# Kernel tuning notes

Measured on AMD Instinct MI355X. Metric: run time of the kernel, lower is better.

Reference implementation:

```python
import jax, jax.numpy as jnp
import numpy as np

N = 20000      # nodes / tokens
H = 256        # hidden_size
NH = 8         # num_heads
HD = NH * H    # num_heads * hidden_size = 2048
EPS = 1e-5


def setup_inputs() -> dict:
    key = jax.random.key(0)
    ks = jax.random.split(key, 24)

    def lin_w(k, i, o):
        # xavier-ish scale for a Linear weight stored as [in, out]
        return jax.random.normal(k, (i, o), jnp.float32) * (1.0 / np.sqrt(i))

    inp = {
        'q': jax.random.normal(ks[0], (N, H), jnp.float32),
        'k': jax.random.normal(ks[1], (N, H), jnp.float32),
        'v': jax.random.normal(ks[2], (N, H), jnp.float32),
        'layer': 1,
        'Wq1': lin_w(ks[3], H, HD), 'bq1': jnp.zeros((HD,), jnp.float32),
        'Wk1': lin_w(ks[4], H, HD), 'bk1': jnp.zeros((HD,), jnp.float32),
        'Wq2': lin_w(ks[5], H, HD), 'bq2': jnp.zeros((HD,), jnp.float32),
        'Wk2': lin_w(ks[6], H, HD), 'bk2': jnp.zeros((HD,), jnp.float32),
        'Wv':  lin_w(ks[7], H, HD), 'bv':  jnp.zeros((HD,), jnp.float32),
        'ln_g': jnp.ones((HD,), jnp.float32),
        'ln_b': jnp.zeros((HD,), jnp.float32),
        'Wo': lin_w(ks[8], HD, H), 'bo': jnp.zeros((H,), jnp.float32),
        'lq1': jax.random.normal(ks[9], (H,), jnp.float32) * 0.1,
        'lk1': jax.random.normal(ks[10], (H,), jnp.float32) * 0.1,
        'lq2': jax.random.normal(ks[11], (H,), jnp.float32) * 0.1,
        'lk2': jax.random.normal(ks[12], (H,), jnp.float32) * 0.1,
    }
    return inp


def reference(q, k, v, layer, Wq1, bq1, Wk1, bk1, Wq2, bq2, Wk2, bk2,
              Wv, bv, ln_g, ln_b, Wo, bo, lq1, lk1, lq2, lk2):
    # projections: [N, H] -> [N, HD]
    q1 = q @ Wq1 + bq1
    k1 = k @ Wk1 + bk1
    q2 = q @ Wq2 + bq2
    k2 = k @ Wk2 + bk2
    vv = v @ Wv + bv

    # linear attention: K^T V -> [HD, HD]  (dropout is identity in eval mode)
    k1v = k1.T @ vv
    k2v = k2.T @ vv

    # lambda gating (scalars)
    lam1 = jnp.exp(jnp.sum(lq1 * lk1))
    lam2 = jnp.exp(jnp.sum(lq2 * lk2))
    lam_init = 0.8 - 0.6 * jnp.exp(jnp.asarray(-0.3 * layer, jnp.float32))
    lam_full = lam1 - lam2 + lam_init

    # Q @ (K^T V), differential subtraction: [N, HD]
    x = q1 @ k1v - lam_full * (q2 @ k2v)

    # LayerNorm over last dim (biased variance, eps=1e-5, like torch)
    mu = jnp.mean(x, axis=-1, keepdims=True)
    var = jnp.mean(jnp.square(x - mu), axis=-1, keepdims=True)
    x = (x - mu) / jnp.sqrt(var + EPS) * ln_g + ln_b

    x = x * (1.0 - lam_init)
    return x @ Wo + bo  # [N, H]
```

## Files before the change

### kernel.cpp

```cpp
#include <hip/hip_runtime.h>
#include <stdint.h>

typedef __bf16 bf16x8 __attribute__((ext_vector_type(8)));
typedef __bf16 bf16x4v __attribute__((ext_vector_type(4)));
typedef float f32x4 __attribute__((ext_vector_type(4)));
typedef float f32x2 __attribute__((ext_vector_type(2)));
typedef unsigned short u16x4 __attribute__((ext_vector_type(4)));
typedef unsigned short u16x8 __attribute__((ext_vector_type(8)));

#define NTOK 20000
#define NTP  20480
#define HIW  256
#define HD   2048
#define LDKP 66
#define LDS2 72

static __device__ __forceinline__ float bf2f(unsigned short h) {
  union { unsigned u; float f; } c; c.u = ((unsigned)h) << 16;
  return c.f;
}
static __device__ __forceinline__ unsigned short fbits(float x) {
  __bf16 h = (__bf16)x;
  return __builtin_bit_cast(unsigned short, h);
}

#define WRED(x) { x += __shfl_xor(x,32); x += __shfl_xor(x,16); x += __shfl_xor(x,8); \
                  x += __shfl_xor(x,4);  x += __shfl_xor(x,2);  x += __shfl_xor(x,1); }


__global__ __launch_bounds__(256) void k_front(
    const float* __restrict__ kk, const float* __restrict__ vv,
    const float* __restrict__ Wq1, const float* __restrict__ Wk1,
    const float* __restrict__ Wq2, const float* __restrict__ Wk2,
    const float* __restrict__ lq1, const float* __restrict__ lk1,
    const float* __restrict__ lq2, const float* __restrict__ lk2,
    const float* __restrict__ bq1, const float* __restrict__ bk1,
    const float* __restrict__ bq2, const float* __restrict__ bk2,
    const int* __restrict__ layer,
    unsigned short* __restrict__ kT, unsigned short* __restrict__ vT,
    float* __restrict__ skp, float* __restrict__ svp,
    unsigned short* __restrict__ Pc_part, float* __restrict__ scal) {
  __shared__ float SMEM[64][260];
  const int b = blockIdx.x, t = threadIdx.x;

  if (b < 640) {
    const int tile = b >> 1, m = b & 1;
    const float* src = m ? vv : kk;
    unsigned short* dstT = m ? vT : kT;
    float* sump = m ? svp : skp;
    #pragma unroll
    for (int i = 0; i < 16; ++i) {
      int ch = i * 256 + t;
      int row = ch >> 6, c4 = (ch & 63) * 4;
      int gtok = tile * 64 + row;
      f32x4 val = {0.f, 0.f, 0.f, 0.f};
      if (gtok < NTOK) val = *(const f32x4*)&src[(size_t)gtok * HIW + c4];
      *(f32x4*)&SMEM[row][c4] = val;
    }
    __syncthreads();
    float sum = 0.f;
    unsigned short cv[64];
    #pragma unroll
    for (int tok = 0; tok < 64; ++tok) {
      float x = SMEM[tok][t];
      sum += x;
      cv[tok] = fbits(x);
    }
    sump[tile * 256 + t] = sum;
    size_t base = (size_t)t * NTP + tile * 64;
    #pragma unroll
    for (int s = 0; s < 8; ++s)
      *(u16x8*)&dstT[base + s * 8] = *(const u16x8*)&cv[s * 8];
  } else if (b < 768) {
    unsigned short* Ak = (unsigned short*)SMEM;
    unsigned short* Bk = Ak + 128 * LDKP;
    const int idx = b - 640;
    const int pair = idx >> 6, rem = idx & 63;
    const int z = rem & 15, by = (rem >> 4) & 1, bx = (rem >> 5) & 1;
    const int i0 = bx * 128, j0 = by * 128;
    const int lane = t & 63, wave = t >> 6;
    const int wr = (wave >> 1) * 64, wc = (wave & 1) * 64;
    const int r15 = lane & 15, kg = (lane >> 4) * 8;
    const float* Wa = pair ? Wq2 : Wq1;
    const float* Wb = pair ? Wk2 : Wk1;
    f32x4 acc[4][4];
    #pragma unroll
    for (int m = 0; m < 4; ++m)
      #pragma unroll
      for (int n = 0; n < 4; ++n) acc[m][n] = (f32x4){0.f, 0.f, 0.f, 0.f};
    const int srow = t >> 1, sh = (t & 1) * 32;
    for (int kt = 0; kt < 2; ++kt) {
      const int kb = z * 128 + kt * 64 + sh;
      __syncthreads();
      #pragma unroll
      for (int c = 0; c < 8; ++c) {
        f32x4 a = *(const f32x4*)&Wa[(size_t)(i0 + srow) * HD + kb + c * 4];
        f32x4 bb = *(const f32x4*)&Wb[(size_t)(j0 + srow) * HD + kb + c * 4];
        bf16x4v oa, ob;
        #pragma unroll
        for (int u = 0; u < 4; ++u) { oa[u] = (__bf16)a[u]; ob[u] = (__bf16)bb[u]; }
        *(bf16x4v*)&Ak[srow * LDKP + sh + c * 4] = oa;
        *(bf16x4v*)&Bk[srow * LDKP + sh + c * 4] = ob;
      }
      __syncthreads();
      #pragma unroll
      for (int ks = 0; ks < 2; ++ks) {
        const int ko = ks * 32 + kg;
        bf16x8 ah[4], bh[4];
        #pragma unroll
        for (int m = 0; m < 4; ++m)
          ah[m] = *(const bf16x8*)&Ak[(wr + m * 16 + r15) * LDKP + ko];
        #pragma unroll
        for (int n = 0; n < 4; ++n)
          bh[n] = *(const bf16x8*)&Bk[(wc + n * 16 + r15) * LDKP + ko];
        #pragma unroll
        for (int m = 0; m < 4; ++m)
          #pragma unroll
          for (int n = 0; n < 4; ++n)
            acc[m][n] = __builtin_amdgcn_mfma_f32_16x16x32_bf16(ah[m], bh[n], acc[m][n], 0, 0, 0);
      }
    }
    const int rg = (lane >> 4) * 4;
    unsigned short* Pp = Pc_part + (size_t)(pair * 16 + z) * 65536;
    #pragma unroll
    for (int m = 0; m < 4; ++m)
      #pragma unroll
      for (int n = 0; n < 4; ++n)
        #pragma unroll
        for (int r = 0; r < 4; ++r)
          Pp[(i0 + wr + m * 16 + rg + r) * 256 + (j0 + wc + n * 16 + r15)] = fbits(acc[m][n][r]);
  } else {
    float* red = (float*)SMEM;
    float p1 = lq1[t] * lk1[t], p2 = lq2[t] * lk2[t];
    float d1 = 0.f, d2 = 0.f;
    #pragma unroll
    for (int u = 0; u < 8; ++u) {
      d1 += bq1[t * 8 + u] * bk1[t * 8 + u];
      d2 += bq2[t * 8 + u] * bk2[t * 8 + u];
    }
    WRED(p1); WRED(p2); WRED(d1); WRED(d2);
    int w = t >> 6;
    if ((t & 63) == 0) { red[w] = p1; red[4 + w] = p2; red[8 + w] = d1; red[12 + w] = d2; }
    __syncthreads();
    if (t == 0) {
      float s1 = red[0] + red[1] + red[2] + red[3];
      float s2 = red[4] + red[5] + red[6] + red[7];
      float dd1 = red[8] + red[9] + red[10] + red[11];
      float dd2 = red[12] + red[13] + red[14] + red[15];
      float li = 0.8f - 0.6f * expf(-0.3f * (float)layer[0]);
      float lam = expf(s1) - expf(s2) + li;
      scal[0] = lam; scal[1] = -lam; scal[2] = 1.0f - li; scal[3] = li;
      scal[4] = dd1 - lam * dd2;
    }
  }
}

__global__ __launch_bounds__(512) void k_mid(
    const unsigned short* __restrict__ kT, const unsigned short* __restrict__ vT,
    float* __restrict__ S, const unsigned short* __restrict__ Pc_part,
    const float* __restrict__ skp, const float* __restrict__ svp,
    float* __restrict__ Pc, float* __restrict__ sk, float* __restrict__ sv,
    const float* __restrict__ Wk1, const float* __restrict__ Wk2,
    const float* __restrict__ Wq1, const float* __restrict__ Wq2,
    const float* __restrict__ bq1, const float* __restrict__ bq2,
    const float* __restrict__ bk1, const float* __restrict__ bk2,
    const float* __restrict__ scal, float* __restrict__ gc, float* __restrict__ uc) {
  __shared__ unsigned short SB[2 * 2 * 128 * LDS2];
  const int b = blockIdx.x, t = threadIdx.x;

  if (b < 256) {
    const int z = b & 63, by = (b >> 6) & 1, bx = (b >> 7) & 1;
    const int i0 = bx * 128, j0 = by * 128;
    const int tok0 = z * 320;
    const int lane = t & 63, wave = t >> 6;
    const int wr = (wave >> 1) * 32, wc = (wave & 1) * 64;
    const int r15 = lane & 15, kg = (lane >> 4) * 8;
    const int m = t >> 8;
    const int local = t & 255;
    const int row2 = local >> 1;
    const int koff = (local & 1) * 32;
    const unsigned short* srcT = m ? vT : kT;
    const size_t rbase = (size_t)((m ? j0 : i0) + row2) * NTP + tok0 + koff;
    const int lds_off = m * 128 * LDS2 + row2 * LDS2 + koff;

    f32x4 acc[2][4];
    #pragma unroll
    for (int mm = 0; mm < 2; ++mm)
      #pragma unroll
      for (int n = 0; n < 4; ++n) acc[mm][n] = (f32x4){0.f, 0.f, 0.f, 0.f};
    u16x8 rA[4], rB[4];

#define LOADT(R, KT)                                                          \
    { _Pragma("unroll")                                                       \
      for (int c = 0; c < 4; ++c)                                             \
        R[c] = *(const u16x8*)&srcT[rbase + (KT) * 64 + c * 8]; }
#define WRITET(BUF, R)                                                        \
    { unsigned short* d = &SB[(BUF) * 2 * 128 * LDS2 + lds_off];              \
      _Pragma("unroll")                                                       \
      for (int c = 0; c < 4; ++c) *(u16x8*)&d[c * 8] = R[c]; }

    LOADT(rA, 0)
    WRITET(0, rA)
    LOADT(rB, 1)
    asm volatile("s_waitcnt lgkmcnt(0)" ::: "memory");
    __builtin_amdgcn_s_barrier();

    #pragma unroll
    for (int kt = 0; kt < 5; ++kt) {
      const unsigned short* Ab = &SB[(kt & 1) * 2 * 128 * LDS2];
      const unsigned short* Bb = Ab + 128 * LDS2;
      __builtin_amdgcn_s_setprio(1);
      #pragma unroll
      for (int ks = 0; ks < 2; ++ks) {
        const int ko = ks * 32 + kg;
        bf16x8 ah[2], bh[4];
        #pragma unroll
        for (int mm = 0; mm < 2; ++mm)
          ah[mm] = *(const bf16x8*)&Ab[(wr + mm * 16 + r15) * LDS2 + ko];
        #pragma unroll
        for (int n = 0; n < 4; ++n)
          bh[n] = *(const bf16x8*)&Bb[(wc + n * 16 + r15) * LDS2 + ko];
        #pragma unroll
        for (int mm = 0; mm < 2; ++mm)
          #pragma unroll
          for (int n = 0; n < 4; ++n)
            acc[mm][n] = __builtin_amdgcn_mfma_f32_16x16x32_bf16(ah[mm], bh[n], acc[mm][n], 0, 0, 0);
      }
      __builtin_amdgcn_s_setprio(0);
      if (kt < 4) {
        if ((kt & 1) == 0) {
          WRITET(1, rB)
          if (kt + 2 <= 4) LOADT(rA, kt + 2)
        } else {
          WRITET(0, rA)
          if (kt + 2 <= 4) LOADT(rB, kt + 2)
        }
      }
      asm volatile("s_waitcnt lgkmcnt(0)" ::: "memory");
      __builtin_amdgcn_s_barrier();
    }
#undef LOADT
#undef WRITET
    const int rg = (lane >> 4) * 4;
    #pragma unroll
    for (int mm = 0; mm < 2; ++mm)
      #pragma unroll
      for (int n = 0; n < 4; ++n)
        #pragma unroll
        for (int r = 0; r < 4; ++r)
          atomicAdd(&S[(i0 + wr + mm * 16 + rg + r) * 256 + (j0 + wc + n * 16 + r15)],
                    acc[mm][n][r]);
  } else if (b < 288) {
    if (t < 256) {
      size_t idx = (size_t)(b - 256) * 2048 + t * 8;
      float s1[8] = {}, s2[8] = {};
      #pragma unroll 2
      for (int z = 0; z < 16; ++z) {
        u16x8 ha = *(const u16x8*)&Pc_part[(size_t)z * 65536 + idx];
        u16x8 hb = *(const u16x8*)&Pc_part[(size_t)(16 + z) * 65536 + idx];
        #pragma unroll
        for (int u = 0; u < 8; ++u) { s1[u] += bf2f(ha[u]); s2[u] += bf2f(hb[u]); }
      }
      float lam = scal[0];
      #pragma unroll
      for (int u = 0; u < 8; ++u) Pc[idx + u] = s1[u] - lam * s2[u];
    }
  } else if (b < 290) {
    if (t < 256) {
      const float* src = (b == 288) ? skp : svp;
      float s = 0.f;
      for (int z = 0; z < 320; ++z) s += src[z * 256 + t];
      if (b == 288) sk[t] = s; else sv[t] = s;
    }
  } else {
    if (t < 256) {
      int bb = b - 290, lane = t & 63, w = t >> 6;
      bool dogc = bb < 16;
      const float* A1 = dogc ? Wk1 : Wq1;
      const float* A2 = dogc ? Wk2 : Wq2;
      const float* x1 = dogc ? bq1 : bk1;
      const float* x2 = dogc ? bq2 : bk2;
      float* outv = dogc ? gc : uc;
      float lam = scal[0];
      int rb = (bb & 15) * 16 + w * 4;
      for (int q2 = 0; q2 < 4; ++q2) {
        int row = rb + q2;
        float s1 = 0.f, s2 = 0.f;
        #pragma unroll
        for (int c = 0; c < 8; ++c) {
          int kk2 = c * 256 + lane * 4;
          f32x4 a1 = *(const f32x4*)&A1[(size_t)row * HD + kk2];
          f32x4 a2 = *(const f32x4*)&A2[(size_t)row * HD + kk2];
          f32x4 v1 = *(const f32x4*)&x1[kk2];
          f32x4 v2 = *(const f32x4*)&x2[kk2];
          #pragma unroll
          for (int u = 0; u < 4; ++u) { s1 += a1[u] * v1[u]; s2 += a2[u] * v2[u]; }
        }
        WRED(s1); WRED(s2);
        if (lane == 0) outv[row] = s1 - lam * s2;
      }
    }
  }
}

__global__ __launch_bounds__(256) void k_ac(
    const float* __restrict__ Pc, const float* __restrict__ S,
    const float* __restrict__ gc, const float* __restrict__ sk,
    float* __restrict__ Ac, float* __restrict__ tc, float* __restrict__ rv,
    float* __restrict__ scal) {
  int b = blockIdx.x, t = threadIdx.x;
  if (b < 32) {
    __shared__ float Pt[32][68];
    __shared__ float St[64][68];
    int i0 = (b >> 2) * 32, j0 = (b & 3) * 64;
    int ti = t >> 5, tj = t & 31;
    float acc[4][2] = {};
    for (int kt = 0; kt < 256; kt += 64) {
      __syncthreads();
      {
        int rr = t >> 3, c8 = (t & 7) * 8;
        *(f32x4*)&Pt[rr][c8] = *(const f32x4*)&Pc[(i0 + rr) * 256 + kt + c8];
        *(f32x4*)&Pt[rr][c8 + 4] = *(const f32x4*)&Pc[(i0 + rr) * 256 + kt + c8 + 4];
      }
      {
        int rr = t >> 2, c16 = (t & 3) * 16;
        #pragma unroll
        for (int c = 0; c < 4; ++c)
          *(f32x4*)&St[rr][c16 + c * 4] = *(const f32x4*)&S[(kt + rr) * 256 + j0 + c16 + c * 4];
      }
      __syncthreads();
      #pragma unroll 8
      for (int k2 = 0; k2 < 64; ++k2) {
        float a[4];
        #pragma unroll
        for (int u = 0; u < 4; ++u) a[u] = Pt[ti * 4 + u][k2];
        f32x2 b2 = *(const f32x2*)&St[k2][tj * 2];
        #pragma unroll
        for (int u = 0; u < 4; ++u) { acc[u][0] += a[u] * b2[0]; acc[u][1] += a[u] * b2[1]; }
      }
    }
    #pragma unroll
    for (int u = 0; u < 4; ++u) {
      Ac[(i0 + ti * 4 + u) * 256 + j0 + tj * 2] = acc[u][0];
      Ac[(i0 + ti * 4 + u) * 256 + j0 + tj * 2 + 1] = acc[u][1];
    }
  } else if (b == 32) {
    int lane = t & 63, w = t >> 6;
    f32x4 sk4 = *(const f32x4*)&sk[lane * 4];
    for (int ii = 0; ii < 64; ++ii) {
      int i = w * 64 + ii;
      f32x4 p4 = *(const f32x4*)&Pc[i * 256 + lane * 4];
      float s = p4[0] * sk4[0] + p4[1] * sk4[1] + p4[2] * sk4[2] + p4[3] * sk4[3];
      WRED(s);
      if (lane == 0) tc[i] = s;
    }
  } else {
    float s0 = 0.f, s1 = 0.f, s2 = 0.f, s3 = 0.f;
    #pragma unroll 4
    for (int i = 0; i < 256; i += 4) {
      s0 += gc[i] * S[i * 256 + t];
      s1 += gc[i + 1] * S[(i + 1) * 256 + t];
      s2 += gc[i + 2] * S[(i + 2) * 256 + t];
      s3 += gc[i + 3] * S[(i + 3) * 256 + t];
    }
    rv[t] = (s0 + s1) + (s2 + s3);
    if (t < 64) {
      f32x4 g4 = *(const f32x4*)&gc[t * 4];
      f32x4 sk4 = *(const f32x4*)&sk[t * 4];
      float a = g4[0] * sk4[0] + g4[1] * sk4[1] + g4[2] * sk4[2] + g4[3] * sk4[3];
      WRED(a);
      if (t == 0) scal[5] = a;
    }
  }
}

__global__ __launch_bounds__(256) void k_gc(
    const float* __restrict__ Ac, const float* __restrict__ Wv,
    const float* __restrict__ tc, const float* __restrict__ uc,
    const float* __restrict__ sv, const float* __restrict__ rv,
    const float* __restrict__ bv, const float* __restrict__ scal,
    float* __restrict__ Gc, float* __restrict__ cc) {
  __shared__ float At[64][68];
  __shared__ float Bt[64][132];
  __shared__ float svr[256], rvr[256];
  int t = threadIdx.x;
  int i0 = blockIdx.x * 64, j0 = blockIdx.y * 128;
  int ti = t >> 5, tj = t & 31;
  svr[t] = sv[t]; rvr[t] = rv[t];
  float acc[8][4] = {};
  f32x4 swa = {0.f, 0.f, 0.f, 0.f}, sca = {0.f, 0.f, 0.f, 0.f};
  for (int kt = 0; kt < 256; kt += 64) {
    __syncthreads();
    {
      int rr = t >> 2, c16 = (t & 3) * 16;
      #pragma unroll
      for (int c = 0; c < 4; ++c)
        *(f32x4*)&At[rr][c16 + c * 4] = *(const f32x4*)&Ac[(i0 + rr) * 256 + kt + c16 + c * 4];
    }
    {
      int rr = t >> 2, c32 = (t & 3) * 32;
      #pragma unroll
      for (int c = 0; c < 8; ++c)
        *(f32x4*)&Bt[rr][c32 + c * 4] = *(const f32x4*)&Wv[(size_t)(kt + rr) * HD + j0 + c32 + c * 4];
    }
    __syncthreads();
    #pragma unroll 8
    for (int k2 = 0; k2 < 64; ++k2) {
      float a[8];
      #pragma unroll
      for (int u = 0; u < 8; ++u) a[u] = At[ti * 8 + u][k2];
      f32x4 b = *(const f32x4*)&Bt[k2][tj * 4];
      float svk = svr[kt + k2], rvk = rvr[kt + k2];
      swa += b * svk; sca += b * rvk;
      #pragma unroll
      for (int u = 0; u < 8; ++u)
        #pragma unroll
        for (int v = 0; v < 4; ++v) acc[u][v] += a[u] * b[v];
    }
  }
  int j = j0 + tj * 4;
  f32x4 bv4 = *(const f32x4*)&bv[j];
  f32x4 wnb;
  #pragma unroll
  for (int v = 0; v < 4; ++v) wnb[v] = swa[v] + 20000.0f * bv4[v];
  if (blockIdx.x == 0 && ti == 0) {
    float ac = scal[5], dc = scal[4];
    f32x4 ccv;
    #pragma unroll
    for (int v = 0; v < 4; ++v) ccv[v] = sca[v] + ac * bv4[v] + dc * wnb[v];
    *(f32x4*)&cc[j] = ccv;
  }
  #pragma unroll
  for (int u = 0; u < 8; ++u) {
    int i = i0 + ti * 8 + u;
    float tci = tc[i], uci = uc[i];
    f32x4 o;
    #pragma unroll
    for (int v = 0; v < 4; ++v)
      o[v] = acc[u][v] + tci * bv4[v] + uci * wnb[v];
    *(f32x4*)&Gc[(size_t)i * HD + j] = o;
  }
}

__global__ __launch_bounds__(256) void k_post(
    const float* __restrict__ Gc, const float* __restrict__ cc,
    const float* __restrict__ Wo, const float* __restrict__ g,
    const float* __restrict__ lnb, const float* __restrict__ scal_c,
    unsigned short* __restrict__ Bt2, float* __restrict__ M_part,
    float* __restrict__ Hc_part, float* __restrict__ scal) {
  __shared__ float SMEM[8768];
  int b = blockIdx.x, t = threadIdx.x;
  if (b < 17) {
    int lane = t & 63, w = t >> 6;
    if (b < 16) {
      int rb = b * 16 + w * 4;
      for (int q2 = 0; q2 < 4; ++q2) {
        int row = rb + q2;
        float s1 = 0.f, s2 = 0.f;
        #pragma unroll
        for (int c = 0; c < 8; ++c) {
          int kk2 = c * 256 + lane * 4;
          f32x4 g4 = *(const f32x4*)&Gc[(size_t)row * HD + kk2];
          f32x4 c4v = *(const f32x4*)&cc[kk2];
          #pragma unroll
          for (int u = 0; u < 4; ++u) { s1 += g4[u]; s2 += g4[u] * c4v[u]; }
        }
        WRED(s1); WRED(s2);
        if (lane == 0) {
          int base = ((256 + (row >> 5)) * 64 + ((row >> 3) & 3) * 16) * 8 + (row & 7);
          Bt2[base] = fbits(s1 * (1.0f / 2048.0f));
          Bt2[base + 8] = fbits(s2);
        }
      }
    } else {
      float s1 = 0.f, s2 = 0.f;
      #pragma unroll
      for (int c = 0; c < 2; ++c) {
        f32x4 v = *(const f32x4*)&cc[t * 8 + c * 4];
        #pragma unroll
        for (int u = 0; u < 4; ++u) { s1 += v[u]; s2 += v[u] * v[u]; }
      }
      WRED(s1); WRED(s2);
      if ((t & 63) == 0) { SMEM[t >> 6] = s1; SMEM[4 + (t >> 6)] = s2; }
      __syncthreads();
      if (t == 0) {
        scal[6] = SMEM[4] + SMEM[5] + SMEM[6] + SMEM[7];
        scal[7] = (SMEM[0] + SMEM[1] + SMEM[2] + SMEM[3]) * (1.0f / 2048.0f);
      }
      for (int idx = t; idx < 14 * 256; idx += 256) {
        int ci = idx >> 8, kk2 = idx & 255;
        int col = 514 + ci;
        Bt2[((256 + (kk2 >> 5)) * 64 + ((kk2 >> 3) & 3) * 16 + (col & 15)) * 8 + (kk2 & 7)] = 0;
      }
    }
  } else if (b < 81) {
    float (*Gi)[68] = (float(*)[68])SMEM;
    float (*Gj)[69] = (float(*)[69])(SMEM + 64 * 68);
    int idx = b - 17;
    int bx = idx & 3, by = (idx >> 2) & 3, z = idx >> 4;
    int i0 = bx * 64, j0 = by * 64;
    int ti = t >> 5, tj = t & 31;
    float acc[8][2] = {};
    for (int kt = 0; kt < 512; kt += 64) {
      int kb = z * 512 + kt;
      __syncthreads();
      {
        int rr = t >> 2, c16 = (t & 3) * 16;
        #pragma unroll
        for (int c = 0; c < 4; ++c) {
          *(f32x4*)&Gi[rr][c16 + c * 4] = *(const f32x4*)&Gc[(size_t)(i0 + rr) * HD + kb + c16 + c * 4];
          *(f32x4*)&Gj[rr][c16 + c * 4] = *(const f32x4*)&Gc[(size_t)(j0 + rr) * HD + kb + c16 + c * 4];
        }
      }
      __syncthreads();
      #pragma unroll 8
      for (int k2 = 0; k2 < 64; ++k2) {
        float a[8];
        #pragma unroll
        for (int u = 0; u < 8; ++u) a[u] = Gi[ti * 8 + u][k2];
        float b0 = Gj[tj * 2][k2], b1 = Gj[tj * 2 + 1][k2];
        #pragma unroll
        for (int u = 0; u < 8; ++u) { acc[u][0] += a[u] * b0; acc[u][1] += a[u] * b1; }
      }
    }
    #pragma unroll
    for (int u = 0; u < 8; ++u) {
      M_part[(size_t)z * 65536 + (i0 + ti * 8 + u) * 256 + j0 + tj * 2] = acc[u][0];
      M_part[(size_t)z * 65536 + (i0 + ti * 8 + u) * 256 + j0 + tj * 2 + 1] = acc[u][1];
    }
  } else {
    float (*At)[68] = (float(*)[68])SMEM;
    float (*Bt)[68] = (float(*)[68])(SMEM + 32 * 68);
    int idx = b - 81;
    int bx = idx % 9, rem = idx / 9, by = rem & 3, z = rem >> 2;
    int i0 = bx * 32, j0 = by * 64;
    float s2 = scal_c[2];
    int ti = t >> 5, tj = t & 31;
    float acc[4][2] = {};
    for (int kt = 0; kt < 512; kt += 64) {
      int kb = z * 512 + kt;
      __syncthreads();
      {
        int rr = t >> 3, c8 = (t & 7) * 8, gi = i0 + rr;
        #pragma unroll
        for (int h = 0; h < 8; h += 4) {
          f32x4 g4 = *(const f32x4*)&g[kb + c8 + h];
          f32x4 a;
          if (gi < 256) {
            f32x4 gg = *(const f32x4*)&Gc[(size_t)gi * HD + kb + c8 + h];
            #pragma unroll
            for (int u = 0; u < 4; ++u) a[u] = gg[u] * g4[u];
          } else if (gi == 256) {
            a = g4;
          } else if (gi == 257) {
            f32x4 c4v = *(const f32x4*)&cc[kb + c8 + h];
            #pragma unroll
            for (int u = 0; u < 4; ++u) a[u] = c4v[u] * g4[u];
          } else if (gi == 258) {
            a = *(const f32x4*)&lnb[kb + c8 + h];
          } else {
            a = (f32x4){0.f, 0.f, 0.f, 0.f};
          }
          *(f32x4*)&At[rr][c8 + h] = a;
        }
      }
      {
        int rr = t >> 2, c16 = (t & 3) * 16;
        #pragma unroll
        for (int c = 0; c < 4; ++c) {
          f32x4 bb = *(const f32x4*)&Wo[(size_t)(kb + rr) * 256 + j0 + c16 + c * 4];
          #pragma unroll
          for (int u = 0; u < 4; ++u) bb[u] *= s2;
          *(f32x4*)&Bt[rr][c16 + c * 4] = bb;
        }
      }
      __syncthreads();
      #pragma unroll 8
      for (int k2 = 0; k2 < 64; ++k2) {
        float a[4];
        #pragma unroll
        for (int u = 0; u < 4; ++u) a[u] = At[ti * 4 + u][k2];
        f32x2 b2 = *(const f32x2*)&Bt[k2][tj * 2];
        #pragma unroll
        for (int u = 0; u < 4; ++u) { acc[u][0] += a[u] * b2[0]; acc[u][1] += a[u] * b2[1]; }
      }
    }
    #pragma unroll
    for (int u = 0; u < 4; ++u) {
      Hc_part[(size_t)z * 73728 + (i0 + ti * 4 + u) * 256 + j0 + tj * 2] = acc[u][0];
      Hc_part[(size_t)z * 73728 + (i0 + ti * 4 + u) * 256 + j0 + tj * 2 + 1] = acc[u][1];
    }
  }
}

__global__ __launch_bounds__(256) void k_red2(
    const float* __restrict__ M_part, const float* __restrict__ Hc_part,
    const float* __restrict__ bo, unsigned short* __restrict__ Bt2,
    float* __restrict__ wbar, float* __restrict__ hcv, float* __restrict__ bcv) {
  int bi = blockIdx.x, z2 = blockIdx.y, t = threadIdx.x;
  if (z2 == 2) {
    if (bi != 0) return;
    float s0 = 0.f, s1 = 0.f, s2 = 0.f;
    #pragma unroll
    for (int z = 0; z < 4; ++z) {
      s0 += Hc_part[(size_t)z * 73728 + 256 * 256 + t];
      s1 += Hc_part[(size_t)z * 73728 + 257 * 256 + t];
      s2 += Hc_part[(size_t)z * 73728 + 258 * 256 + t];
    }
    wbar[t] = s0; hcv[t] = s1; bcv[t] = s2 + bo[t];
    return;
  }
  __shared__ unsigned short T[64][256];
  const float* src = z2 ? Hc_part : M_part;
  const size_t sp = z2 ? 73728 : 65536;
  const int base = z2 ? 256 : 0;
  for (int ii = 0; ii < 64; ++ii) {
    int i = bi * 64 + ii;
    float s = 0.f;
    #pragma unroll
    for (int z = 0; z < 4; ++z) s += src[z * sp + i * 256 + t];
    T[ii][t] = fbits(s);
  }
  __syncthreads();
  const int col = base + t;
  #pragma unroll
  for (int c = 0; c < 64; c += 8) {
    u16x8 o;
    #pragma unroll
    for (int u = 0; u < 8; ++u) o[u] = T[c + u][t];
    int kk0 = bi * 64 + c;
    int addr = (((col >> 4) * 8 + (kk0 >> 5)) * 64 + ((kk0 >> 3) & 3) * 16 + (col & 15)) * 8;
    *(u16x8*)&Bt2[addr] = o;
  }
}

__global__ __launch_bounds__(256) void k_out(
    const float* __restrict__ q, const unsigned short* __restrict__ Bt2,
    const float* __restrict__ hcv, const float* __restrict__ wbar,
    const float* __restrict__ bcv, const float* __restrict__ scal,
    float* __restrict__ out) {
  __shared__ unsigned short As[32 * 264];
  __shared__ float sqp[2][32];
  __shared__ float muL[32], m2L[32];
  const int t = threadIdx.x, lane = t & 63, wave = t >> 6;
  const int row0 = blockIdx.x * 32;
  const int r15 = lane & 15, kg = lane >> 4;
  {
    int r = t >> 3;
    #pragma unroll
    for (int ci = 0; ci < 8; ++ci) {
      int col = ci * 32 + (t & 7) * 4;
      f32x4 v = *(const f32x4*)&q[(size_t)(row0 + r) * HIW + col];
      bf16x4v o;
      #pragma unroll
      for (int u = 0; u < 4; ++u) o[u] = (__bf16)v[u];
      *(bf16x4v*)&As[r * 264 + col] = o;
    }
  }
  __syncthreads();
  const int wc = wave * 128;
  const unsigned short* bbase = Bt2 + (size_t)(wave * 8) * 4096 + (size_t)lane * 8;
  f32x4 acc[2][9];
  #pragma unroll
  for (int m = 0; m < 2; ++m)
    #pragma unroll
    for (int n = 0; n < 9; ++n) acc[m][n] = (f32x4){0.f, 0.f, 0.f, 0.f};
  __builtin_amdgcn_s_setprio(1);
  #pragma unroll
  for (int ko = 0; ko < 8; ++ko) {
    bf16x8 af0 = *(const bf16x8*)&As[r15 * 264 + ko * 32 + kg * 8];
    bf16x8 af1 = *(const bf16x8*)&As[(16 + r15) * 264 + ko * 32 + kg * 8];
    #pragma unroll
    for (int ni = 0; ni < 9; ++ni) {
      if (ni == 8 && wave != 3) continue;
      bf16x8 bfr = *(const bf16x8*)&bbase[ni * 4096 + ko * 512];
      acc[0][ni] = __builtin_amdgcn_mfma_f32_16x16x32_bf16(af0, bfr, acc[0][ni], 0, 0, 0);
      acc[1][ni] = __builtin_amdgcn_mfma_f32_16x16x32_bf16(af1, bfr, acc[1][ni], 0, 0, 0);
    }
  }
  __builtin_amdgcn_s_setprio(0);
  if (wave < 2) {
    #pragma unroll
    for (int m = 0; m < 2; ++m)
      #pragma unroll
      for (int r = 0; r < 4; ++r) {
        int rowl = m * 16 + kg * 4 + r;
        float p = 0.f;
        #pragma unroll
        for (int ni = 0; ni < 8; ++ni) {
          int col = wc + ni * 16 + r15;
          p += acc[m][ni][r] * bf2f(As[rowl * 264 + col]);
        }
        p += __shfl_xor(p, 1); p += __shfl_xor(p, 2);
        p += __shfl_xor(p, 4); p += __shfl_xor(p, 8);
        if (r15 == 0) sqp[wave][rowl] = p;
      }
  }
  if (wave == 3) {
    #pragma unroll
    for (int m = 0; m < 2; ++m)
      #pragma unroll
      for (int r = 0; r < 4; ++r) {
        int rowl = m * 16 + kg * 4 + r;
        if (r15 == 0) muL[rowl] = acc[m][8][r];
        if (r15 == 1) m2L[rowl] = acc[m][8][r];
      }
  }
  __syncthreads();
  if (wave >= 2) {
    const float css = scal[6], cbar = scal[7];
    #pragma unroll
    for (int m = 0; m < 2; ++m)
      #pragma unroll
      for (int r = 0; r < 4; ++r) {
        int rowl = m * 16 + kg * 4 + r;
        float mu = muL[rowl] + cbar;
        float ss = sqp[0][rowl] + sqp[1][rowl] + 2.0f * m2L[rowl] + css;
        float var = ss * (1.0f / 2048.0f) - mu * mu;
        float rstd = rsqrtf(var + 1e-5f);
        int grow = row0 + rowl;
        #pragma unroll
        for (int ni = 0; ni < 8; ++ni) {
          int oc = (wc - 256) + ni * 16 + r15;
          float zv = acc[m][ni][r] + hcv[oc];
          out[(size_t)grow * HIW + oc] = rstd * (zv - mu * wbar[oc]) + bcv[oc];
        }
      }
  }
}

extern "C" void kernel_launch(void* const* d_in, const int* in_sizes, int n_in,
                              void* d_out, int out_size, void* d_ws, size_t ws_size,
                              hipStream_t stream) {
  const float* q   = (const float*)d_in[0];
  const float* k   = (const float*)d_in[1];
  const float* v   = (const float*)d_in[2];
  const int* layer = (const int*)d_in[3];
  const float* Wq1 = (const float*)d_in[4];  const float* bq1 = (const float*)d_in[5];
  const float* Wk1 = (const float*)d_in[6];  const float* bk1 = (const float*)d_in[7];
  const float* Wq2 = (const float*)d_in[8];  const float* bq2 = (const float*)d_in[9];
  const float* Wk2 = (const float*)d_in[10]; const float* bk2 = (const float*)d_in[11];
  const float* Wv  = (const float*)d_in[12]; const float* bv  = (const float*)d_in[13];
  const float* lng = (const float*)d_in[14]; const float* lnb = (const float*)d_in[15];
  const float* Wo  = (const float*)d_in[16]; const float* bo  = (const float*)d_in[17];
  const float* lq1 = (const float*)d_in[18]; const float* lk1 = (const float*)d_in[19];
  const float* lq2 = (const float*)d_in[20]; const float* lk2 = (const float*)d_in[21];

  char* p = (char*)d_ws;
  unsigned short* kT = (unsigned short*)p;
  float* M_part  = (float*)p;
  float* Hc_part = (float*)(p + 1048576);
  unsigned short* Bt2 = (unsigned short*)(p + 1048576 + 1179648);
  p += (size_t)256 * NTP * 2;
  unsigned short* vT = (unsigned short*)p;
  float* Gc = (float*)p;
  p += (size_t)256 * NTP * 2;
  float* skp = (float*)p;     p += (size_t)320 * 256 * 4;
  float* svp = (float*)p;     p += (size_t)320 * 256 * 4;
  unsigned short* Pc_part = (unsigned short*)p; p += (size_t)32 * 65536 * 2;
  float* S  = (float*)p;      p += 65536 * 4;
  float* Pc = (float*)p;      p += 65536 * 4;
  float* sk = (float*)p;      p += 1024;
  float* sv = (float*)p;      p += 1024;
  float* gc = (float*)p;      p += 1024;
  float* uc = (float*)p;      p += 1024;
  float* tc = (float*)p;      p += 1024;
  float* rv = (float*)p;      p += 1024;
  float* cc = (float*)p;      p += 2048 * 4;
  float* Ac = (float*)p;      p += 65536 * 4;
  float* wbar = (float*)p;    p += 1024;
  float* hcv  = (float*)p;    p += 1024;
  float* bcv  = (float*)p;    p += 1024;
  float* scal = (float*)p;    p += 256;

  const dim3 b256(256);
  hipMemsetAsync(S, 0, 65536 * 4, stream);
  k_front<<<dim3(769), b256, 0, stream>>>(k, v, Wq1, Wk1, Wq2, Wk2,
      lq1, lk1, lq2, lk2, bq1, bk1, bq2, bk2, layer, kT, vT, skp, svp, Pc_part, scal);
  k_mid<<<dim3(322), dim3(512), 0, stream>>>(kT, vT, S, Pc_part, skp, svp, Pc, sk, sv,
      Wk1, Wk2, Wq1, Wq2, bq1, bq2, bk1, bk2, scal, gc, uc);
  k_ac<<<dim3(34), b256, 0, stream>>>(Pc, S, gc, sk, Ac, tc, rv, scal);
  k_gc<<<dim3(4, 16), b256, 0, stream>>>(Ac, Wv, tc, uc, sv, rv, bv, scal, Gc, cc);
  k_post<<<dim3(225), b256, 0, stream>>>(Gc, cc, Wo, lng, lnb, scal, Bt2, M_part, Hc_part, scal);
  k_red2<<<dim3(4, 3), b256, 0, stream>>>(M_part, Hc_part, bo, Bt2, wbar, hcv, bcv);
  k_out<<<dim3(625), b256, 0, stream>>>(q, Bt2, hcv, wbar, bcv, scal, (float*)d_out);
}
```

Before: 193.8 us.

## Fold S zeroing into k_front and coalesce k_out epilogue via LDS staging

Replaces the separate hipMemsetAsync of the S accumulator with an extra block in k_front that writes zeros, removing one stream operation and its launch gap. In k_out, waves 2-3 now stage their output accumulators in a shared-memory buffer. All four waves then write the normalized rows with coalesced float4 stores instead of scattered scalar stores from two waves. The extra ~33KB of LDS per block may lower occupancy of k_out.

```diff
diff --git a/kernel.cpp b/kernel.cpp
--- a/kernel.cpp
+++ b/kernel.cpp
@@ -39,7 +39,8 @@
     const int* __restrict__ layer,
     unsigned short* __restrict__ kT, unsigned short* __restrict__ vT,
     float* __restrict__ skp, float* __restrict__ svp,
-    unsigned short* __restrict__ Pc_part, float* __restrict__ scal) {
+    unsigned short* __restrict__ Pc_part, float* __restrict__ scal,
+    float* __restrict__ S) {
   __shared__ float SMEM[64][260];
   const int b = blockIdx.x, t = threadIdx.x;
 
@@ -129,7 +130,7 @@
         #pragma unroll
         for (int r = 0; r < 4; ++r)
           Pp[(i0 + wr + m * 16 + rg + r) * 256 + (j0 + wc + n * 16 + r15)] = fbits(acc[m][n][r]);
-  } else {
+  } else if (b == 768) {
     float* red = (float*)SMEM;
     float p1 = lq1[t] * lk1[t], p2 = lq2[t] * lk2[t];
     float d1 = 0.f, d2 = 0.f;
@@ -152,6 +153,11 @@
       scal[0] = lam; scal[1] = -lam; scal[2] = 1.0f - li; scal[3] = li;
       scal[4] = dd1 - lam * dd2;
     }
+  } else {
+    const f32x4 z4 = {0.f, 0.f, 0.f, 0.f};
+    #pragma unroll
+    for (int i = 0; i < 64; ++i)
+      *(f32x4*)&S[i * 1024 + t * 4] = z4;
   }
 }
 
@@ -640,6 +646,7 @@
     const float* __restrict__ bcv, const float* __restrict__ scal,
     float* __restrict__ out) {
   __shared__ unsigned short As[32 * 264];
+  __shared__ float zbuf[32][260];
   __shared__ float sqp[2][32];
   __shared__ float muL[32], m2L[32];
   const int t = threadIdx.x, lane = t & 63, wave = t >> 6;
@@ -695,37 +702,46 @@
         p += __shfl_xor(p, 4); p += __shfl_xor(p, 8);
         if (r15 == 0) sqp[wave][rowl] = p;
       }
-  }
-  if (wave == 3) {
+  } else {
     #pragma unroll
     for (int m = 0; m < 2; ++m)
       #pragma unroll
       for (int r = 0; r < 4; ++r) {
         int rowl = m * 16 + kg * 4 + r;
-        if (r15 == 0) muL[rowl] = acc[m][8][r];
-        if (r15 == 1) m2L[rowl] = acc[m][8][r];
-      }
+        #pragma unroll
+        for (int ni = 0; ni < 8; ++ni)
+          zbuf[rowl][(wc - 256) + ni * 16 + r15] = acc[m][ni][r];
+      }
+    if (wave == 3) {
+      #pragma unroll
+      for (int m = 0; m < 2; ++m)
+        #pragma unroll
+        for (int r = 0; r < 4; ++r) {
+          int rowl = m * 16 + kg * 4 + r;
+          if (r15 == 0) muL[rowl] = acc[m][8][r];
+          if (r15 == 1) m2L[rowl] = acc[m][8][r];
+        }
+    }
   }
   __syncthreads();
-  if (wave >= 2) {
-    const float css = scal[6], cbar = scal[7];
-    #pragma unroll
-    for (int m = 0; m < 2; ++m)
-      #pragma unroll
-      for (int r = 0; r < 4; ++r) {
-        int rowl = m * 16 + kg * 4 + r;
-        float mu = muL[rowl] + cbar;
-        float ss = sqp[0][rowl] + sqp[1][rowl] + 2.0f * m2L[rowl] + css;
-        float var = ss * (1.0f / 2048.0f) - mu * mu;
-        float rstd = rsqrtf(var + 1e-5f);
-        int grow = row0 + rowl;
-        #pragma unroll
-        for (int ni = 0; ni < 8; ++ni) {
-          int oc = (wc - 256) + ni * 16 + r15;
-          float zv = acc[m][ni][r] + hcv[oc];
-          out[(size_t)grow * HIW + oc] = rstd * (zv - mu * wbar[oc]) + bcv[oc];
-        }
-      }
+  const float css = scal[6], cbar = scal[7];
+  #pragma unroll
+  for (int i = 0; i < 8; ++i) {
+    const int row = i * 4 + wave;
+    const int c4 = lane * 4;
+    float mu = muL[row] + cbar;
+    float ss = sqp[0][row] + sqp[1][row] + 2.0f * m2L[row] + css;
+    float var = ss * (1.0f / 2048.0f) - mu * mu;
+    float rstd = rsqrtf(var + 1e-5f);
+    f32x4 zv = *(const f32x4*)&zbuf[row][c4];
+    f32x4 h4 = *(const f32x4*)&hcv[c4];
+    f32x4 w4 = *(const f32x4*)&wbar[c4];
+    f32x4 b4 = *(const f32x4*)&bcv[c4];
+    f32x4 o;
+    #pragma unroll
+    for (int u = 0; u < 4; ++u)
+      o[u] = rstd * (zv[u] + h4[u] - mu * w4[u]) + b4[u];
+    *(f32x4*)&out[(size_t)(row0 + row) * HIW + c4] = o;
   }
 }
 
@@ -774,9 +790,8 @@
   float* scal = (float*)p;    p += 256;
 
   const dim3 b256(256);
-  hipMemsetAsync(S, 0, 65536 * 4, stream);
-  k_front<<<dim3(769), b256, 0, stream>>>(k, v, Wq1, Wk1, Wq2, Wk2,
-      lq1, lk1, lq2, lk2, bq1, bk1, bq2, bk2, layer, kT, vT, skp, svp, Pc_part, scal);
+  k_front<<<dim3(770), b256, 0, stream>>>(k, v, Wq1, Wk1, Wq2, Wk2,
+      lq1, lk1, lq2, lk2, bq1, bk1, bq2, bk2, layer, kT, vT, skp, svp, Pc_part, scal, S);
   k_mid<<<dim3(322), dim3(512), 0, stream>>>(kT, vT, S, Pc_part, skp, svp, Pc, sk, sv,
       Wk1, Wk2, Wq1, Wq2, bq1, bq2, bk1, bk2, scal, gc, uc);
   k_ac<<<dim3(34), b256, 0, stream>>>(Pc, S, gc, sk, Ac, tc, rv, scal);
```

Result: faster. 180.6 us (-6.8%).
